# Kernel optimization log

Hardware: AMD Instinct MI355X
Metric: run time of the kernel (lower is better)

Reference implementation:

```python
import jax, jax.numpy as jnp
import numpy as np

E = 4; NQ = 144; NL = 2; NH = 16; H = 1024; OUT = 4096; TD = 256
NT = 5; NEL = 10; TOPK = 2
STAGE_Q = (64, 48, 32); STAGE_IMG = (256, 256, 256)
B = 8; LV = 576; LP = 192


def setup_inputs():
    key = jax.random.key(0)
    ks = jax.random.split(key, 16)
    rn = lambda k, s, std=0.02: jax.random.normal(k, s, jnp.float32) * std
    return dict(
        image_embs=jax.random.normal(ks[0], (B, LV, H), jnp.float32),
        physical_prompts=jax.random.normal(ks[1], (B, LP, H), jnp.float32),
        task_ids=jax.random.randint(ks[2], (B,), 0, NT),
        element_ids=jax.random.randint(ks[3], (B,), 0, NEL),
        query=rn(ks[4], (E, NQ, H), 0.01),
        ln1_w=jnp.ones((E, NL, H)), ln1_b=jnp.zeros((E, NL, H)),
        ln1kv_w=jnp.ones((E, NL, H)), ln1kv_b=jnp.zeros((E, NL, H)),
        attn_in_w=rn(ks[5], (E, NL, 3 * H, H)), attn_in_b=jnp.zeros((E, NL, 3 * H)),
        attn_out_w=rn(ks[6], (E, NL, H, H)), attn_out_b=jnp.zeros((E, NL, H)),
        ls1=jnp.full((E, NL, H), 0.1), ls2=jnp.full((E, NL, H), 0.1),
        ln2_w=jnp.ones((E, NL, H)), ln2_b=jnp.zeros((E, NL, H)),
        fc_w=rn(ks[7], (E, NL, 4 * H, H)), fc_b=jnp.zeros((E, NL, 4 * H)),
        proj_w=rn(ks[8], (E, NL, H, 4 * H)), proj_b=jnp.zeros((E, NL, H)),
        outp_w=rn(ks[9], (E, OUT, H)), outp_b=jnp.zeros((E, OUT)),
        task_emb=rn(ks[10], (NT, TD)), elem_emb=rn(ks[11], (NEL, TD)),
        gate_ln_w=jnp.ones((H + 2 * TD,)), gate_ln_b=jnp.zeros((H + 2 * TD,)),
        gate_w=rn(ks[12], (E, H + 2 * TD)), gate_b=jnp.zeros((E,)),
        output_gain=jnp.full((OUT,), 0.3), final_w=jnp.ones((OUT,)),
    )


def _ln(x, w, b, eps=1e-5):
    m = jnp.mean(x, -1, keepdims=True)
    v = jnp.mean((x - m) ** 2, -1, keepdims=True)
    return (x - m) * jax.lax.rsqrt(v + eps) * w + b


def _mha(q, kv, in_w, in_b, out_w, out_b):
    # torch nn.MultiheadAttention with packed in_proj_weight [3H,H]
    d = q.shape[-1]; hd = d // NH
    qp = (q @ in_w[:d].T + in_b[:d]).reshape(q.shape[0], q.shape[1], NH, hd)
    kp = (kv @ in_w[d:2 * d].T + in_b[d:2 * d]).reshape(kv.shape[0], kv.shape[1], NH, hd)
    vp = (kv @ in_w[2 * d:].T + in_b[2 * d:]).reshape(kv.shape[0], kv.shape[1], NH, hd)
    s = jnp.einsum('bqhd,bkhd->bhqk', qp, kp) / np.float32(np.sqrt(hd))
    a = jax.nn.softmax(s, axis=-1)
    o = jnp.einsum('bhqk,bkhd->bqhd', a, vp).reshape(q.shape)
    return o @ out_w.T + out_b


def _pooler(p, z):
    # One AttnPooler expert. z: [B, LV+LP, H]; stages use fixed query/kv splits.
    b = z.shape[0]
    qt = jnp.broadcast_to(p['query'][None], (b, NQ, H))
    qo = 0; io = 0; outs = []
    for sq, si in zip(STAGE_Q, STAGE_IMG):
        x = qt[:, qo:qo + sq]
        kv0 = jnp.concatenate([x, z[:, io:io + si]], axis=1)  # cat_embs fixed across layers
        qo += sq; io += si
        for l in range(NL):
            kvn = _ln(kv0, p['ln1kv_w'][l], p['ln1kv_b'][l])
            a = _mha(_ln(x, p['ln1_w'][l], p['ln1_b'][l]), kvn,
                     p['attn_in_w'][l], p['attn_in_b'][l],
                     p['attn_out_w'][l], p['attn_out_b'][l])
            x = x + p['ls1'][l] * a
            h = _ln(x, p['ln2_w'][l], p['ln2_b'][l])
            h = jax.nn.gelu(h @ p['fc_w'][l].T + p['fc_b'][l], approximate=False)
            x = x + p['ls2'][l] * (h @ p['proj_w'][l].T + p['proj_b'][l])
        outs.append(x)
    y = jnp.concatenate(outs, axis=1)  # [B, NQ, H]
    return y @ p['outp_w'].T + p['outp_b']  # [B, NQ, OUT]


def reference(image_embs, physical_prompts, task_ids, element_ids, query,
              ln1_w, ln1_b, ln1kv_w, ln1kv_b, attn_in_w, attn_in_b,
              attn_out_w, attn_out_b, ls1, ls2, ln2_w, ln2_b, fc_w, fc_b,
              proj_w, proj_b, outp_w, outp_b, task_emb, elem_emb,
              gate_ln_w, gate_ln_b, gate_w, gate_b, output_gain, final_w):
    # Gating
    tg = jnp.take(task_emb, task_ids, axis=0)
    eg = jnp.take(elem_emb, element_ids, axis=0)
    gi = jnp.concatenate([jnp.mean(image_embs, axis=1), tg, eg], axis=-1)
    logits = jnp.clip(_ln(gi, gate_ln_w, gate_ln_b) @ gate_w.T + gate_b, -15.0, 15.0)
    gw = jax.nn.softmax(logits, axis=-1)
    tw, ti = jax.lax.top_k(gw, TOPK)
    tw = tw / (jnp.sum(tw, axis=-1, keepdims=True) + 1e-9)
    gates = jnp.sum(tw[..., None] * jax.nn.one_hot(ti, E, dtype=tw.dtype), axis=1)  # [B,E]
    # Joint feature sequence
    z = jnp.concatenate([image_embs, physical_prompts], axis=1)
    ep = dict(query=query, ln1_w=ln1_w, ln1_b=ln1_b, ln1kv_w=ln1kv_w, ln1kv_b=ln1kv_b,
              attn_in_w=attn_in_w, attn_in_b=attn_in_b, attn_out_w=attn_out_w,
              attn_out_b=attn_out_b, ls1=ls1, ls2=ls2, ln2_w=ln2_w, ln2_b=ln2_b,
              fc_w=fc_w, fc_b=fc_b, proj_w=proj_w, proj_b=proj_b,
              outp_w=outp_w, outp_b=outp_b)
    eo = jax.vmap(lambda p: _pooler(p, z))(ep)  # [E,B,NQ,OUT]
    comb = jnp.einsum('ebqd,be->bqd', eo, gates)
    rms = comb * jax.lax.rsqrt(jnp.mean(comb * comb, axis=-1, keepdims=True) + 1e-6)
    return rms * final_w * output_gain
```

## Files before the change

### kernel.cpp

```cpp
#include <hip/hip_runtime.h>

typedef unsigned short u16;
typedef __bf16 bf16x8 __attribute__((ext_vector_type(8)));
typedef float f32x4 __attribute__((ext_vector_type(4)));

typedef const __attribute__((address_space(1))) void* gp1;
typedef __attribute__((address_space(3))) void* lp3;

__device__ __forceinline__ float bf2f(u16 u){
    union { unsigned int i; float f; } v; v.i = ((unsigned int)u) << 16; return v.f;
}
__device__ __forceinline__ u16 f2bf(float f){
    union { float f; unsigned int i; } v; v.f = f;
    unsigned int u = v.i;
    return (u16)((u + 0x7FFFu + ((u >> 16) & 1u)) >> 16);
}

__device__ __forceinline__ void gload16(const u16* g, const u16* l){
    __builtin_amdgcn_global_load_lds((gp1)(uintptr_t)g, (lp3)(uintptr_t)l, 16, 0, 0);
}

__device__ __forceinline__ float blockSum(float v){
    #pragma unroll
    for (int off = 32; off; off >>= 1) v += __shfl_xor(v, off, 64);
    __shared__ float sm[4];
    const int w = threadIdx.x >> 6;
    __syncthreads();
    if ((threadIdx.x & 63) == 0) sm[w] = v;
    __syncthreads();
    return sm[0] + sm[1] + sm[2] + sm[3];
}

__global__ __launch_bounds__(256)
void cvt_k(const float* __restrict__ in, u16* __restrict__ out, long long n)
{
    const long long stride = (long long)gridDim.x * 256 * 8;
    for (long long i = ((long long)blockIdx.x * 256 + threadIdx.x) * 8; i < n; i += stride) {
        float4 a = *(const float4*)(in + i);
        float4 b = *(const float4*)(in + i + 4);
        uint4 o;
        o.x = (unsigned)f2bf(a.x) | ((unsigned)f2bf(a.y) << 16);
        o.y = (unsigned)f2bf(a.z) | ((unsigned)f2bf(a.w) << 16);
        o.z = (unsigned)f2bf(b.x) | ((unsigned)f2bf(b.y) << 16);
        o.w = (unsigned)f2bf(b.z) | ((unsigned)f2bf(b.w) << 16);
        *(uint4*)(out + i) = o;
    }
}

__global__ __launch_bounds__(256)
void img_mean_k(const float* __restrict__ img, float* __restrict__ part)
{
    const int b = blockIdx.x >> 5, c = blockIdx.x & 31;
    const int t = threadIdx.x;
    const float* p = img + ((size_t)b * 576 + (size_t)c * 18) * 1024 + t * 4;
    float4 s = make_float4(0.f, 0.f, 0.f, 0.f);
    #pragma unroll
    for (int r = 0; r < 18; r++) {
        float4 v = *(const float4*)(p + (size_t)r * 1024);
        s.x += v.x; s.y += v.y; s.z += v.z; s.w += v.w;
    }
    *(float4*)(part + (size_t)blockIdx.x * 1024 + t * 4) = s;
}

template<int EPI, int TM>
__global__ __launch_bounds__(256)
void gemm_big(const u16* __restrict__ A, long long a_zo, long long a_zi, int lda,
              const u16* __restrict__ W, long long w_zo, long long w_zi, int ldw,
              void* __restrict__ Cv, long long c_zo, long long c_zi, int ldc,
              const float* __restrict__ bias, long long b_zo,
              const float* __restrict__ ls, long long ls_zo,
              int M, int N, int K, int Zi)
{
    constexpr int MI = TM / 32;
    __shared__ u16 As[TM * 64];
    __shared__ u16 Ws[128 * 64];
    const int z  = blockIdx.z;
    const int zo = z / Zi, zi = z - zo * Zi;
    const u16* Az = A + (long long)zo * a_zo + (long long)zi * a_zi;
    const u16* Wz = W + (long long)zo * w_zo + (long long)zi * w_zi;
    const int m0 = blockIdx.y * TM, n0 = blockIdx.x * 128;
    const int t = threadIdx.x;
    const int lane = t & 63, wid = t >> 6;
    const int wm = (wid >> 1) * (TM / 2), wn = (wid & 1) * 64;
    const int qd = lane >> 4, ml = lane & 15;
    const int srow = t >> 3, scol = (t & 7) * 8;

    f32x4 acc[MI][4];
    #pragma unroll
    for (int i = 0; i < MI; i++)
        #pragma unroll
        for (int j = 0; j < 4; j++) acc[i][j] = (f32x4){0.f, 0.f, 0.f, 0.f};

    int arow[MI];
    #pragma unroll
    for (int i = 0; i < MI; i++) {
        int r = m0 + i * 32 + srow; arow[i] = (r < M) ? r : (M - 1);
    }
    int wrow[4];
    #pragma unroll
    for (int i = 0; i < 4; i++) {
        int r = n0 + i * 32 + srow; wrow[i] = (r < N) ? r : (N - 1);
    }

    for (int k0 = 0; k0 < K; k0 += 64) {
        #pragma unroll
        for (int i = 0; i < MI; i++)
            gload16(Az + (size_t)arow[i] * lda + k0 + scol, &As[(i * 32 + wid * 8) * 64]);
        #pragma unroll
        for (int i = 0; i < 4; i++)
            gload16(Wz + (size_t)wrow[i] * ldw + k0 + scol, &Ws[(i * 32 + wid * 8) * 64]);
        __syncthreads();
        #pragma unroll
        for (int kk = 0; kk < 64; kk += 32) {
            bf16x8 af[MI], bfr[4];
            #pragma unroll
            for (int i = 0; i < MI; i++)
                af[i] = __builtin_bit_cast(bf16x8, *(const uint4*)&As[(wm + 16*i + ml) * 64 + kk + qd * 8]);
            #pragma unroll
            for (int j = 0; j < 4; j++)
                bfr[j] = __builtin_bit_cast(bf16x8, *(const uint4*)&Ws[(wn + 16*j + ml) * 64 + kk + qd * 8]);
            #pragma unroll
            for (int i = 0; i < MI; i++)
                #pragma unroll
                for (int j = 0; j < 4; j++)
                    acc[i][j] = __builtin_amdgcn_mfma_f32_16x16x32_bf16(af[i], bfr[j], acc[i][j], 0, 0, 0);
        }
        __syncthreads();
    }

    const float* bz = bias ? bias + (long long)zo * b_zo : nullptr;
    const float* lz = (EPI == 3) ? ls + (long long)zo * ls_zo : nullptr;
    const long long coff = (long long)zo * c_zo + (long long)zi * c_zi;

    #pragma unroll
    for (int i = 0; i < MI; i++) {
        #pragma unroll
        for (int j = 0; j < 4; j++) {
            const int nn = n0 + wn + 16 * j + ml;
            if (nn >= N) continue;
            const float bv = bz ? bz[nn] : 0.f;
            if (EPI == 2) {
                const int mmb = m0 + wm + 16 * i + qd * 4;
                u16* C = (u16*)Cv + coff + (size_t)nn * ldc + mmb;
                if (mmb + 3 < M) {
                    u16 tmp[4];
                    #pragma unroll
                    for (int r = 0; r < 4; r++) tmp[r] = f2bf(acc[i][j][r] + bv);
                    *(uint2*)C = make_uint2((unsigned)tmp[0] | ((unsigned)tmp[1] << 16),
                                            (unsigned)tmp[2] | ((unsigned)tmp[3] << 16));
                } else {
                    #pragma unroll
                    for (int r = 0; r < 4; r++)
                        if (mmb + r < M) C[r] = f2bf(acc[i][j][r] + bv);
                }
            } else {
                const float lsv = (EPI == 3) ? lz[nn] : 0.f;
                #pragma unroll
                for (int r = 0; r < 4; r++) {
                    const int mm = m0 + wm + 16 * i + qd * 4 + r;
                    if (mm >= M) continue;
                    float v = acc[i][j][r];
                    if (EPI == 0) {
                        ((u16*)Cv + coff)[(size_t)mm * ldc + nn] = f2bf(v + bv);
                    } else if (EPI == 3) {
                        float* C = (float*)Cv + coff;
                        const size_t idx = (size_t)mm * ldc + nn;
                        C[idx] = C[idx] + lsv * (v + bv);
                    } else {
                        float x = v + bv;
                        float g = 0.5f * x * (1.f + erff(x * 0.70710678118654752f));
                        ((u16*)Cv + coff)[(size_t)mm * ldc + nn] = f2bf(g);
                    }
                }
            }
        }
    }
}

template<int EPI, int WF32>
__global__ __launch_bounds__(256)
void gemm_k(const u16* __restrict__ A, long long a_zo, long long a_zi, int lda,
            const void* __restrict__ W, long long w_zo, long long w_zi, int ldw,
            void* __restrict__ Cv, long long c_zo, long long c_zi, int ldc,
            const float* __restrict__ bias, long long b_zo,
            const float* __restrict__ ls, long long ls_zo,
            int M, int N, int K, int Zi)
{
    __shared__ u16 As[64][72];
    __shared__ u16 Ws[64][72];
    const int z  = blockIdx.z;
    const int zo = z / Zi, zi = z - zo * Zi;
    const u16* Az = A + (long long)zo * a_zo + (long long)zi * a_zi;
    const long long wbase = (long long)zo * w_zo + (long long)zi * w_zi;
    const int m0 = blockIdx.y * 64, n0 = blockIdx.x * 64;
    const int t = threadIdx.x;
    const int lrow = t >> 2, lcol = (t & 3) * 16;
    const int lane = t & 63, wid = t >> 6;
    const int wm = (wid >> 1) * 32, wn = (wid & 1) * 32;
    const int qd = lane >> 4, ml = lane & 15;

    f32x4 acc[2][2];
    #pragma unroll
    for (int i = 0; i < 2; i++)
        #pragma unroll
        for (int j = 0; j < 2; j++) acc[i][j] = (f32x4){0.f, 0.f, 0.f, 0.f};

    const bool arv = (m0 + lrow) < M;
    const bool wrv = (n0 + lrow) < N;
    const u16* ap = Az + (size_t)(m0 + lrow) * lda + lcol;

    for (int k0 = 0; k0 < K; k0 += 64) {
        {
            uint4 av0 = make_uint4(0u,0u,0u,0u), av1 = make_uint4(0u,0u,0u,0u);
            if (arv && (k0 + lcol) < K) {
                av0 = *(const uint4*)(ap + k0);
                av1 = *(const uint4*)(ap + k0 + 8);
            }
            *(uint4*)&As[lrow][lcol]     = av0;
            *(uint4*)&As[lrow][lcol + 8] = av1;
        }
        if (WF32) {
            const float* wp = (const float*)W + wbase + (size_t)(n0 + lrow) * ldw + lcol;
            const bool ok = wrv && (k0 + lcol) < K;
            u16 tmp[16];
            #pragma unroll
            for (int c = 0; c < 16; c += 4) {
                float4 f = make_float4(0.f,0.f,0.f,0.f);
                if (ok) f = *(const float4*)(wp + k0 + c);
                tmp[c+0] = f2bf(f.x); tmp[c+1] = f2bf(f.y);
                tmp[c+2] = f2bf(f.z); tmp[c+3] = f2bf(f.w);
            }
            unsigned pk[8];
            #pragma unroll
            for (int c = 0; c < 8; c++)
                pk[c] = (unsigned)tmp[2*c] | ((unsigned)tmp[2*c+1] << 16);
            *(uint4*)&Ws[lrow][lcol]     = make_uint4(pk[0],pk[1],pk[2],pk[3]);
            *(uint4*)&Ws[lrow][lcol + 8] = make_uint4(pk[4],pk[5],pk[6],pk[7]);
        } else {
            const u16* wp = (const u16*)W + wbase + (size_t)(n0 + lrow) * ldw + lcol;
            uint4 wv0 = make_uint4(0u,0u,0u,0u), wv1 = make_uint4(0u,0u,0u,0u);
            if (wrv && (k0 + lcol) < K) {
                wv0 = *(const uint4*)(wp + k0);
                wv1 = *(const uint4*)(wp + k0 + 8);
            }
            *(uint4*)&Ws[lrow][lcol]     = wv0;
            *(uint4*)&Ws[lrow][lcol + 8] = wv1;
        }
        __syncthreads();
        #pragma unroll
        for (int kk = 0; kk < 64; kk += 32) {
            bf16x8 af[2], bfr[2];
            #pragma unroll
            for (int i = 0; i < 2; i++) {
                af[i]  = __builtin_bit_cast(bf16x8, *(const uint4*)&As[wm + 16*i + ml][kk + qd*8]);
                bfr[i] = __builtin_bit_cast(bf16x8, *(const uint4*)&Ws[wn + 16*i + ml][kk + qd*8]);
            }
            #pragma unroll
            for (int i = 0; i < 2; i++)
                #pragma unroll
                for (int j = 0; j < 2; j++)
                    acc[i][j] = __builtin_amdgcn_mfma_f32_16x16x32_bf16(af[i], bfr[j], acc[i][j], 0, 0, 0);
        }
        __syncthreads();
    }

    const float* bz = (EPI != 1 && bias) ? bias + (long long)zo * b_zo : nullptr;
    const float* lz = (EPI == 3) ? ls + (long long)zo * ls_zo : nullptr;

    #pragma unroll
    for (int i = 0; i < 2; i++) {
        #pragma unroll
        for (int j = 0; j < 2; j++) {
            const int nn = n0 + wn + 16*j + ml;
            if (nn >= N) continue;
            float bv = 0.f;
            if (EPI != 1 && bz) bv = bz[nn];
            float lsv = 0.f;
            if (EPI == 3) lsv = lz[nn];
            #pragma unroll
            for (int r = 0; r < 4; r++) {
                const int mm = m0 + wm + 16*i + qd*4 + r;
                if (mm >= M) continue;
                float v = acc[i][j][r];
                if (EPI == 0) {
                    u16* C = (u16*)Cv + (long long)zo * c_zo + (long long)zi * c_zi;
                    C[(size_t)mm * ldc + nn] = f2bf(v + bv);
                } else if (EPI == 1) {
                    float* C = (float*)Cv + (long long)zo * c_zo + (long long)zi * c_zi;
                    C[(size_t)mm * ldc + nn] = v * 0.125f;
                } else if (EPI == 2) {
                    u16* C = (u16*)Cv + (long long)zo * c_zo + (long long)zi * c_zi;
                    C[(size_t)nn * ldc + mm] = f2bf(v + bv);
                } else if (EPI == 3) {
                    float* C = (float*)Cv + (long long)zo * c_zo + (long long)zi * c_zi;
                    const size_t idx = (size_t)mm * ldc + nn;
                    C[idx] = C[idx] + lsv * (v + bv);
                } else {
                    u16* C = (u16*)Cv + (long long)zo * c_zo + (long long)zi * c_zi;
                    float x = v + bv;
                    float g = 0.5f * x * (1.f + erff(x * 0.70710678118654752f));
                    C[(size_t)mm * ldc + nn] = f2bf(g);
                }
            }
        }
    }
}

template<int INF32>
__global__ __launch_bounds__(256)
void ln_k(const void* __restrict__ in, u16* __restrict__ out,
          const float* __restrict__ w, const float* __restrict__ b,
          long long wz, int rows_per_e)
{
    const int row = blockIdx.x;
    const int e = row / rows_per_e;
    const int t = threadIdx.x;
    float x[4];
    if (INF32) {
        const float* p = (const float*)in + (size_t)row * 1024;
        #pragma unroll
        for (int j = 0; j < 4; j++) x[j] = p[t + 256*j];
    } else {
        const u16* p = (const u16*)in + (size_t)row * 1024;
        #pragma unroll
        for (int j = 0; j < 4; j++) x[j] = bf2f(p[t + 256*j]);
    }
    float s = x[0] + x[1] + x[2] + x[3];
    s = blockSum(s);
    const float m = s * (1.f / 1024.f);
    float vs = 0.f;
    #pragma unroll
    for (int j = 0; j < 4; j++) { float d = x[j] - m; vs += d * d; }
    vs = blockSum(vs);
    const float rs = rsqrtf(vs * (1.f / 1024.f) + 1e-5f);
    const float* we = w + (long long)e * wz;
    const float* be = b + (long long)e * wz;
    u16* o = out + (size_t)row * 1024;
    #pragma unroll
    for (int j = 0; j < 4; j++) {
        const int h = t + 256*j;
        o[h] = f2bf((x[j] - m) * rs * we[h] + be[h]);
    }
}

__global__ __launch_bounds__(256)
void softmax_k(const float* __restrict__ S, u16* __restrict__ P, int kl, int nrows)
{
    const int r = blockIdx.x * 4 + (threadIdx.x >> 6);
    const int lane = threadIdx.x & 63;
    if (r >= nrows) return;
    const float* s = S + (size_t)r * kl;
    float v[6];
    int cnt = 0;
    float mx = -3.4e38f;
    for (int i = lane; i < kl; i += 64) { float tv = s[i]; v[cnt++] = tv; mx = fmaxf(mx, tv); }
    #pragma unroll
    for (int off = 32; off; off >>= 1) mx = fmaxf(mx, __shfl_xor(mx, off, 64));
    float sum = 0.f;
    for (int i = 0; i < cnt; i++) { v[i] = expf(v[i] - mx); sum += v[i]; }
    #pragma unroll
    for (int off = 32; off; off >>= 1) sum += __shfl_xor(sum, off, 64);
    const float inv = 1.f / sum;
    u16* p = P + (size_t)r * kl;
    cnt = 0;
    for (int i = lane; i < kl; i += 64) p[i] = f2bf(v[cnt++] * inv);
}

__global__ __launch_bounds__(256)
void prep_k(const float* __restrict__ query, const float* __restrict__ img, const float* __restrict__ prm,
            u16* __restrict__ KV0, float* __restrict__ X,
            int sq, int qo, int io, int kl)
{
    const int idx = blockIdx.x;
    const int e = idx / (8 * kl);
    const int rem = idx - e * 8 * kl;
    const int b = rem / kl;
    const int k = rem - b * kl;
    const int t = threadIdx.x;
    const float* src;
    if (k < sq) src = query + ((size_t)e * 144 + qo + k) * 1024;
    else {
        const int zr = io + (k - sq);
        src = (zr < 576) ? img + ((size_t)b * 576 + zr) * 1024
                         : prm + ((size_t)b * 192 + (zr - 576)) * 1024;
    }
    const float4 d = *(const float4*)(src + t * 4);
    u16* dst = KV0 + (((size_t)(e * 8 + b) * kl) + k) * 1024 + t * 4;
    unsigned p0 = (unsigned)f2bf(d.x) | ((unsigned)f2bf(d.y) << 16);
    unsigned p1 = (unsigned)f2bf(d.z) | ((unsigned)f2bf(d.w) << 16);
    *(uint2*)dst = make_uint2(p0, p1);
    if (k < sq) {
        float* xd = X + (((size_t)(e * 8 + b) * sq) + k) * 1024 + t * 4;
        *(float4*)xd = d;
    }
}

__global__ __launch_bounds__(256)
void copy_y_k(const float* __restrict__ X, u16* __restrict__ Y, int sq, int qoff)
{
    const int idx = blockIdx.x;
    const int e = idx / (8 * sq);
    const int rem = idx - e * 8 * sq;
    const int b = rem / sq;
    const int q = rem - b * sq;
    const int t = threadIdx.x;
    const float* xs = X + (((size_t)(e * 8 + b) * sq) + q) * 1024;
    u16* yd = Y + (((size_t)(e * 8 + b) * 144) + qoff + q) * 1024;
    #pragma unroll
    for (int j = 0; j < 4; j++) { const int h = t + 256*j; yd[h] = f2bf(xs[h]); }
}

__global__ __launch_bounds__(256)
void gate_k(const float* __restrict__ part, const int* __restrict__ tids, const int* __restrict__ eids,
            const float* __restrict__ temb, const float* __restrict__ eemb,
            const float* __restrict__ glw, const float* __restrict__ glb,
            const float* __restrict__ gw, const float* __restrict__ gb,
            float* __restrict__ gates)
{
    const int b = blockIdx.x;
    const int t = threadIdx.x;
    __shared__ float gi[1536];
    for (int h = t; h < 1024; h += 256) {
        float s = 0.f;
        #pragma unroll
        for (int c = 0; c < 32; c++) s += part[((size_t)b * 32 + c) * 1024 + h];
        gi[h] = s * (1.f / 576.f);
    }
    {
        const int ti = tids[b], ei = eids[b];
        gi[1024 + t] = temb[ti * 256 + t];
        gi[1280 + t] = eemb[ei * 256 + t];
    }
    __syncthreads();
    float s = 0.f;
    for (int i = t; i < 1536; i += 256) s += gi[i];
    s = blockSum(s);
    const float m = s * (1.f / 1536.f);
    float vs = 0.f;
    for (int i = t; i < 1536; i += 256) { float d = gi[i] - m; vs += d * d; }
    vs = blockSum(vs);
    const float rs = rsqrtf(vs * (1.f / 1536.f) + 1e-5f);
    __shared__ float logit[4];
    for (int e = 0; e < 4; e++) {
        float p = 0.f;
        for (int i = t; i < 1536; i += 256)
            p += ((gi[i] - m) * rs * glw[i] + glb[i]) * gw[e * 1536 + i];
        p = blockSum(p);
        if (t == 0) logit[e] = p + gb[e];
    }
    __syncthreads();
    if (t == 0) {
        float lg[4], ex[4];
        float mx = -1e30f;
        for (int e = 0; e < 4; e++) { lg[e] = fminf(15.f, fmaxf(-15.f, logit[e])); mx = fmaxf(mx, lg[e]); }
        float sum = 0.f;
        for (int e = 0; e < 4; e++) { ex[e] = expf(lg[e] - mx); sum += ex[e]; }
        for (int e = 0; e < 4; e++) ex[e] /= sum;
        int i1 = 0;
        for (int e = 1; e < 4; e++) if (ex[e] > ex[i1]) i1 = e;
        int i2 = -1;
        for (int e = 0; e < 4; e++) if (e != i1 && (i2 < 0 || ex[e] > ex[i2])) i2 = e;
        const float denom = ex[i1] + ex[i2] + 1e-9f;
        float g[4] = {0.f, 0.f, 0.f, 0.f};
        g[i1] = ex[i1] / denom;
        g[i2] = ex[i2] / denom;
        for (int e = 0; e < 4; e++) gates[b * 4 + e] = g[e];
    }
}

__global__ __launch_bounds__(256)
void comb_k(const u16* __restrict__ EO, const float* __restrict__ gates,
            const float* __restrict__ fw, const float* __restrict__ og,
            float* __restrict__ out)
{
    const int bq = blockIdx.x;
    const int b = bq / 144;
    const int t = threadIdx.x;
    float g[4];
    #pragma unroll
    for (int e = 0; e < 4; e++) g[e] = gates[b * 4 + e];
    float c[16];
    float ss = 0.f;
    #pragma unroll
    for (int j = 0; j < 16; j++) {
        const int o = t + 256 * j;
        float v = 0.f;
        #pragma unroll
        for (int e = 0; e < 4; e++)
            v += g[e] * bf2f(EO[((size_t)e * 1152 + bq) * 4096 + o]);
        c[j] = v;
        ss += v * v;
    }
    ss = blockSum(ss);
    const float rs = rsqrtf(ss * (1.f / 4096.f) + 1e-6f);
    #pragma unroll
    for (int j = 0; j < 16; j++) {
        const int o = t + 256 * j;
        out[(size_t)bq * 4096 + o] = c[j] * rs * fw[o] * og[o];
    }
}

extern "C" void kernel_launch(void* const* d_in, const int* in_sizes, int n_in,
                              void* d_out, int out_size, void* d_ws, size_t ws_size,
                              hipStream_t stream)
{
    const float* img  = (const float*)d_in[0];
    const float* prm  = (const float*)d_in[1];
    const int*   tids = (const int*)d_in[2];
    const int*   eids = (const int*)d_in[3];
    const float* query= (const float*)d_in[4];
    const float* ln1w = (const float*)d_in[5];
    const float* ln1b = (const float*)d_in[6];
    const float* lkw  = (const float*)d_in[7];
    const float* lkb  = (const float*)d_in[8];
    const float* aiw  = (const float*)d_in[9];
    const float* aib  = (const float*)d_in[10];
    const float* aow  = (const float*)d_in[11];
    const float* aob  = (const float*)d_in[12];
    const float* ls1  = (const float*)d_in[13];
    const float* ls2  = (const float*)d_in[14];
    const float* l2w  = (const float*)d_in[15];
    const float* l2b  = (const float*)d_in[16];
    const float* fcw  = (const float*)d_in[17];
    const float* fcb  = (const float*)d_in[18];
    const float* pjw  = (const float*)d_in[19];
    const float* pjb  = (const float*)d_in[20];
    const float* opw  = (const float*)d_in[21];
    const float* opb  = (const float*)d_in[22];
    const float* temb = (const float*)d_in[23];
    const float* eemb = (const float*)d_in[24];
    const float* glw  = (const float*)d_in[25];
    const float* glb  = (const float*)d_in[26];
    const float* gww  = (const float*)d_in[27];
    const float* gbb  = (const float*)d_in[28];
    const float* og   = (const float*)d_in[29];
    const float* fwv  = (const float*)d_in[30];
    float* out = (float*)d_out;
    (void)in_sizes; (void)n_in; (void)out_size; (void)ws_size;

    char* ws = (char*)d_ws;
    size_t off = 0;
    auto alloc = [&](size_t bytes) -> char* {
        char* p = ws + off;
        off += (bytes + 255) & ~(size_t)255;
        return p;
    };
    float* GATES = (float*)alloc(128);
    float* IPART = (float*)alloc(1048576);
    u16*  AIWB = (u16*) alloc(50331648);
    u16*  AOWB = (u16*) alloc(16777216);
    u16*  FCWB = (u16*) alloc(67108864);
    u16*  PJWB = (u16*) alloc(67108864);
    u16*  OPWB = (u16*) alloc(33554432);
    u16*  KV0 = (u16*) alloc(20971520);
    u16*  KVN = (u16*) alloc(20971520);
    u16*  KP  = (u16*) alloc(20971520);
    u16*  VT  = (u16*) alloc(20971520);
    float* S  = (float*)alloc(41943040);
    u16*  QN  = (u16*) alloc(4194304);
    u16*  QP  = (u16*) alloc(4194304);
    u16*  AO  = (u16*) alloc(4194304);
    float* X  = (float*)alloc(8388608);
    u16*  H4  = (u16*) alloc(16777216);
    u16*  Y   = (u16*) alloc(9437184);
    u16*  EO  = (u16*) alloc(37748736);

    const long long HH = 1024LL * 1024LL;

    cvt_k<<<2048, 256, 0, stream>>>(aiw, AIWB, 25165824LL);
    cvt_k<<<2048, 256, 0, stream>>>(aow, AOWB, 8388608LL);
    cvt_k<<<2048, 256, 0, stream>>>(fcw, FCWB, 33554432LL);
    cvt_k<<<2048, 256, 0, stream>>>(pjw, PJWB, 33554432LL);
    cvt_k<<<2048, 256, 0, stream>>>(opw, OPWB, 16777216LL);

    img_mean_k<<<256, 256, 0, stream>>>(img, IPART);
    gate_k<<<8, 256, 0, stream>>>(IPART, tids, eids, temb, eemb, glw, glb, gww, gbb, GATES);

    const int SQ[3] = {64, 48, 32};
    const int IO[3] = {0, 256, 512};
    const int QO[3] = {0, 64, 112};
    const int KL[3] = {320, 304, 288};

    for (int s = 0; s < 3; s++) {
        const int sq = SQ[s], kl = KL[s], qo = QO[s], io = IO[s];
        const int Msq = 8 * sq;
        const int Mkl = 8 * kl;
        prep_k<<<4 * 8 * kl, 256, 0, stream>>>(query, img, prm, KV0, X, sq, qo, io, kl);
        for (int l = 0; l < 2; l++) {
            ln_k<0><<<4 * 8 * kl, 256, 0, stream>>>(KV0, KVN, lkw + l*1024, lkb + l*1024, 2048, 8 * kl);
            ln_k<1><<<4 * 8 * sq, 256, 0, stream>>>(X,   QN,  ln1w + l*1024, ln1b + l*1024, 2048, 8 * sq);
            gemm_big<0,64><<<dim3(8, Msq/64, 4), 256, 0, stream>>>(
                QN, (long long)Msq * 1024, 0, 1024,
                AIWB + (long long)l * 3 * HH, 6 * HH, 0, 1024,
                QP, (long long)Msq * 1024, 0, 1024,
                aib + l * 3072, 6144,
                nullptr, 0, Msq, 1024, 1024, 1);
            gemm_big<0,128><<<dim3(8, Mkl/128, 4), 256, 0, stream>>>(
                KVN, (long long)Mkl * 1024, 0, 1024,
                AIWB + (long long)l * 3 * HH + HH, 6 * HH, 0, 1024,
                KP, (long long)Mkl * 1024, 0, 1024,
                aib + l * 3072 + 1024, 6144,
                nullptr, 0, Mkl, 1024, 1024, 1);
            gemm_big<2,128><<<dim3(8, (kl + 127)/128, 32), 256, 0, stream>>>(
                KVN, (long long)8 * kl * 1024, (long long)kl * 1024, 1024,
                AIWB + (long long)l * 3 * HH + 2 * HH, 6 * HH, 0, 1024,
                VT, (long long)8 * 1024 * kl, (long long)1024 * kl, kl,
                aib + l * 3072 + 2048, 6144,
                nullptr, 0, kl, 1024, 1024, 8);
            gemm_k<1,0><<<dim3((kl + 63)/64, 1, 512), 256, 0, stream>>>(
                QP, (long long)sq * 1024, 64, 1024,
                KP, (long long)kl * 1024, 64, 1024,
                S, (long long)16 * sq * kl, (long long)sq * kl, kl,
                nullptr, 0, nullptr, 0, sq, kl, 64, 16);
            {
                const int nrows = 4 * 8 * 16 * sq;
                softmax_k<<<(nrows + 3)/4, 256, 0, stream>>>(S, KVN, kl, nrows);
            }
            gemm_k<0,0><<<dim3(1, 1, 512), 256, 0, stream>>>(
                KVN, (long long)16 * sq * kl, (long long)sq * kl, kl,
                VT, (long long)1024 * kl, (long long)64 * kl, kl,
                AO, (long long)sq * 1024, 64, 1024,
                nullptr, 0, nullptr, 0, sq, 64, kl, 16);
            gemm_big<3,64><<<dim3(8, Msq/64, 4), 256, 0, stream>>>(
                AO, (long long)Msq * 1024, 0, 1024,
                AOWB + (long long)l * HH, 2 * HH, 0, 1024,
                X, (long long)Msq * 1024, 0, 1024,
                aob + l * 1024, 2048,
                ls1 + l * 1024, 2048,
                Msq, 1024, 1024, 1);
            ln_k<1><<<4 * 8 * sq, 256, 0, stream>>>(X, QN, l2w + l*1024, l2b + l*1024, 2048, 8 * sq);
            gemm_big<4,128><<<dim3(32, Msq/128, 4), 256, 0, stream>>>(
                QN, (long long)Msq * 1024, 0, 1024,
                FCWB + (long long)l * 4 * HH, 8 * HH, 0, 1024,
                H4, (long long)Msq * 4096, 0, 4096,
                fcb + l * 4096, 8192,
                nullptr, 0, Msq, 4096, 1024, 1);
            gemm_big<3,64><<<dim3(8, Msq/64, 4), 256, 0, stream>>>(
                H4, (long long)Msq * 4096, 0, 4096,
                PJWB + (long long)l * 4 * HH, 8 * HH, 0, 4096,
                X, (long long)Msq * 1024, 0, 1024,
                pjb + l * 1024, 2048,
                ls2 + l * 1024, 2048,
                Msq, 1024, 4096, 1);
        }
        copy_y_k<<<4 * 8 * sq, 256, 0, stream>>>(X, Y, sq, qo);
    }
    gemm_big<0,128><<<dim3(32, 9, 4), 256, 0, stream>>>(
        Y, 1152LL * 1024, 0, 1024,
        OPWB, 4096LL * 1024, 0, 1024,
        EO, 1152LL * 4096, 0, 4096,
        opb, 4096,
        nullptr, 0, 1152, 4096, 1024, 1);
    comb_k<<<1152, 256, 0, stream>>>(EO, GATES, fwv, og, out);
}
```

Before: 2.964 ms.

## Double-buffer and swizzle gemm_big LDS, fuse K and V projections into one GEMM

gemm_big now double-buffers its LDS tiles so the global-to-LDS loads for the next K-slice overlap the MFMA work on the current one. It also XOR-swizzles the LDS column layout to cut bank conflicts on fragment reads. The separate K-projection and transposed V-projection launches become a single N=2048 GEMM whose new epilogue (EPI 5) writes KP row-major and VT transposed per batch. Dead epilogue branches and the fp32-weight path in gemm_k are removed; the trade-off is double the LDS per block, which can lower occupancy, and the fused epilogue writes without bounds checks, so it relies on Mkl being a multiple of the tile size.

```diff
diff --git a/kernel.cpp b/kernel.cpp
--- a/kernel.cpp
+++ b/kernel.cpp
@@ -72,8 +72,8 @@
               int M, int N, int K, int Zi)
 {
     constexpr int MI = TM / 32;
-    __shared__ u16 As[TM * 64];
-    __shared__ u16 Ws[128 * 64];
+    __shared__ u16 As[2][TM * 64];
+    __shared__ u16 Ws[2][128 * 64];
     const int z  = blockIdx.z;
     const int zo = z / Zi, zi = z - zo * Zi;
     const u16* Az = A + (long long)zo * a_zo + (long long)zi * a_zi;
@@ -83,7 +83,8 @@
     const int lane = t & 63, wid = t >> 6;
     const int wm = (wid >> 1) * (TM / 2), wn = (wid & 1) * 64;
     const int qd = lane >> 4, ml = lane & 15;
-    const int srow = t >> 3, scol = (t & 7) * 8;
+    const int srow = t >> 3;
+    const int scol = (((t & 7) ^ (srow & 7)) << 3);
 
     f32x4 acc[MI][4];
     #pragma unroll
@@ -102,23 +103,37 @@
         int r = n0 + i * 32 + srow; wrow[i] = (r < N) ? r : (N - 1);
     }
 
-    for (int k0 = 0; k0 < K; k0 += 64) {
+    auto stage = [&](int buf, int k0){
         #pragma unroll
         for (int i = 0; i < MI; i++)
-            gload16(Az + (size_t)arow[i] * lda + k0 + scol, &As[(i * 32 + wid * 8) * 64]);
+            gload16(Az + (size_t)arow[i] * lda + k0 + scol, &As[buf][(i * 32 + wid * 8) * 64]);
         #pragma unroll
         for (int i = 0; i < 4; i++)
-            gload16(Wz + (size_t)wrow[i] * ldw + k0 + scol, &Ws[(i * 32 + wid * 8) * 64]);
-        __syncthreads();
+            gload16(Wz + (size_t)wrow[i] * ldw + k0 + scol, &Ws[buf][(i * 32 + wid * 8) * 64]);
+    };
+
+    const int NT = K >> 6;
+    stage(0, 0);
+    __syncthreads();
+    for (int it = 0; it < NT; ++it) {
+        if (it + 1 < NT) stage((it + 1) & 1, (it + 1) << 6);
+        const u16* Ab = As[it & 1];
+        const u16* Wb = Ws[it & 1];
         #pragma unroll
         for (int kk = 0; kk < 64; kk += 32) {
             bf16x8 af[MI], bfr[4];
             #pragma unroll
-            for (int i = 0; i < MI; i++)
-                af[i] = __builtin_bit_cast(bf16x8, *(const uint4*)&As[(wm + 16*i + ml) * 64 + kk + qd * 8]);
-            #pragma unroll
-            for (int j = 0; j < 4; j++)
-                bfr[j] = __builtin_bit_cast(bf16x8, *(const uint4*)&Ws[(wn + 16*j + ml) * 64 + kk + qd * 8]);
+            for (int i = 0; i < MI; i++) {
+                const int row = wm + 16 * i + ml;
+                const int ch  = (((qd + (kk >> 3)) ^ (ml & 7)) << 3);
+                af[i] = __builtin_bit_cast(bf16x8, *(const uint4*)&Ab[row * 64 + ch]);
+            }
+            #pragma unroll
+            for (int j = 0; j < 4; j++) {
+                const int row = wn + 16 * j + ml;
+                const int ch  = (((qd + (kk >> 3)) ^ (ml & 7)) << 3);
+                bfr[j] = __builtin_bit_cast(bf16x8, *(const uint4*)&Wb[row * 64 + ch]);
+            }
             #pragma unroll
             for (int i = 0; i < MI; i++)
                 #pragma unroll
@@ -132,6 +147,36 @@
     const float* lz = (EPI == 3) ? ls + (long long)zo * ls_zo : nullptr;
     const long long coff = (long long)zo * c_zo + (long long)zi * c_zi;
 
+    if (EPI == 5) {
+        const int klv = (int)c_zi;
+        u16* KPz = (u16*)Cv + (long long)zo * c_zo;
+        u16* VTz = (u16*)(uintptr_t)(const void*)ls + (long long)zo * ls_zo;
+        #pragma unroll
+        for (int i = 0; i < MI; i++) {
+            #pragma unroll
+            for (int j = 0; j < 4; j++) {
+                const int nn = n0 + wn + 16 * j + ml;
+                const float bv = bz[nn];
+                const int mmb = m0 + wm + 16 * i + qd * 4;
+                if (nn < 1024) {
+                    #pragma unroll
+                    for (int r = 0; r < 4; r++)
+                        KPz[(size_t)(mmb + r) * ldc + nn] = f2bf(acc[i][j][r] + bv);
+                } else {
+                    const int b = mmb / klv;
+                    const int k = mmb - b * klv;
+                    u16 tmp[4];
+                    #pragma unroll
+                    for (int r = 0; r < 4; r++) tmp[r] = f2bf(acc[i][j][r] + bv);
+                    u16* p = VTz + ((size_t)(b * 1024 + (nn - 1024))) * klv + k;
+                    *(uint2*)p = make_uint2((unsigned)tmp[0] | ((unsigned)tmp[1] << 16),
+                                            (unsigned)tmp[2] | ((unsigned)tmp[3] << 16));
+                }
+            }
+        }
+        return;
+    }
+
     #pragma unroll
     for (int i = 0; i < MI; i++) {
         #pragma unroll
@@ -139,38 +184,22 @@
             const int nn = n0 + wn + 16 * j + ml;
             if (nn >= N) continue;
             const float bv = bz ? bz[nn] : 0.f;
-            if (EPI == 2) {
-                const int mmb = m0 + wm + 16 * i + qd * 4;
-                u16* C = (u16*)Cv + coff + (size_t)nn * ldc + mmb;
-                if (mmb + 3 < M) {
-                    u16 tmp[4];
-                    #pragma unroll
-                    for (int r = 0; r < 4; r++) tmp[r] = f2bf(acc[i][j][r] + bv);
-                    *(uint2*)C = make_uint2((unsigned)tmp[0] | ((unsigned)tmp[1] << 16),
-                                            (unsigned)tmp[2] | ((unsigned)tmp[3] << 16));
+            const float lsv = (EPI == 3) ? lz[nn] : 0.f;
+            #pragma unroll
+            for (int r = 0; r < 4; r++) {
+                const int mm = m0 + wm + 16 * i + qd * 4 + r;
+                if (mm >= M) continue;
+                float v = acc[i][j][r];
+                if (EPI == 0) {
+                    ((u16*)Cv + coff)[(size_t)mm * ldc + nn] = f2bf(v + bv);
+                } else if (EPI == 3) {
+                    float* C = (float*)Cv + coff;
+                    const size_t idx = (size_t)mm * ldc + nn;
+                    C[idx] = C[idx] + lsv * (v + bv);
                 } else {
-                    #pragma unroll
-                    for (int r = 0; r < 4; r++)
-                        if (mmb + r < M) C[r] = f2bf(acc[i][j][r] + bv);
-                }
-            } else {
-                const float lsv = (EPI == 3) ? lz[nn] : 0.f;
-                #pragma unroll
-                for (int r = 0; r < 4; r++) {
-                    const int mm = m0 + wm + 16 * i + qd * 4 + r;
-                    if (mm >= M) continue;
-                    float v = acc[i][j][r];
-                    if (EPI == 0) {
-                        ((u16*)Cv + coff)[(size_t)mm * ldc + nn] = f2bf(v + bv);
-                    } else if (EPI == 3) {
-                        float* C = (float*)Cv + coff;
-                        const size_t idx = (size_t)mm * ldc + nn;
-                        C[idx] = C[idx] + lsv * (v + bv);
-                    } else {
-                        float x = v + bv;
-                        float g = 0.5f * x * (1.f + erff(x * 0.70710678118654752f));
-                        ((u16*)Cv + coff)[(size_t)mm * ldc + nn] = f2bf(g);
-                    }
+                    float x = v + bv;
+                    float g = 0.5f * x * (1.f + erff(x * 0.70710678118654752f));
+                    ((u16*)Cv + coff)[(size_t)mm * ldc + nn] = f2bf(g);
                 }
             }
         }
@@ -219,24 +248,7 @@
             *(uint4*)&As[lrow][lcol]     = av0;
             *(uint4*)&As[lrow][lcol + 8] = av1;
         }
-        if (WF32) {
-            const float* wp = (const float*)W + wbase + (size_t)(n0 + lrow) * ldw + lcol;
-            const bool ok = wrv && (k0 + lcol) < K;
-            u16 tmp[16];
-            #pragma unroll
-            for (int c = 0; c < 16; c += 4) {
-                float4 f = make_float4(0.f,0.f,0.f,0.f);
-                if (ok) f = *(const float4*)(wp + k0 + c);
-                tmp[c+0] = f2bf(f.x); tmp[c+1] = f2bf(f.y);
-                tmp[c+2] = f2bf(f.z); tmp[c+3] = f2bf(f.w);
-            }
-            unsigned pk[8];
-            #pragma unroll
-            for (int c = 0; c < 8; c++)
-                pk[c] = (unsigned)tmp[2*c] | ((unsigned)tmp[2*c+1] << 16);
-            *(uint4*)&Ws[lrow][lcol]     = make_uint4(pk[0],pk[1],pk[2],pk[3]);
-            *(uint4*)&Ws[lrow][lcol + 8] = make_uint4(pk[4],pk[5],pk[6],pk[7]);
-        } else {
+        {
             const u16* wp = (const u16*)W + wbase + (size_t)(n0 + lrow) * ldw + lcol;
             uint4 wv0 = make_uint4(0u,0u,0u,0u), wv1 = make_uint4(0u,0u,0u,0u);
             if (wrv && (k0 + lcol) < K) {
@@ -264,42 +276,23 @@
         __syncthreads();
     }
 
-    const float* bz = (EPI != 1 && bias) ? bias + (long long)zo * b_zo : nullptr;
-    const float* lz = (EPI == 3) ? ls + (long long)zo * ls_zo : nullptr;
-
     #pragma unroll
     for (int i = 0; i < 2; i++) {
         #pragma unroll
         for (int j = 0; j < 2; j++) {
             const int nn = n0 + wn + 16*j + ml;
             if (nn >= N) continue;
-            float bv = 0.f;
-            if (EPI != 1 && bz) bv = bz[nn];
-            float lsv = 0.f;
-            if (EPI == 3) lsv = lz[nn];
             #pragma unroll
             for (int r = 0; r < 4; r++) {
                 const int mm = m0 + wm + 16*i + qd*4 + r;
                 if (mm >= M) continue;
                 float v = acc[i][j][r];
-                if (EPI == 0) {
-                    u16* C = (u16*)Cv + (long long)zo * c_zo + (long long)zi * c_zi;
-                    C[(size_t)mm * ldc + nn] = f2bf(v + bv);
-                } else if (EPI == 1) {
+                if (EPI == 1) {
                     float* C = (float*)Cv + (long long)zo * c_zo + (long long)zi * c_zi;
                     C[(size_t)mm * ldc + nn] = v * 0.125f;
-                } else if (EPI == 2) {
-                    u16* C = (u16*)Cv + (long long)zo * c_zo + (long long)zi * c_zi;
-                    C[(size_t)nn * ldc + mm] = f2bf(v + bv);
-                } else if (EPI == 3) {
-                    float* C = (float*)Cv + (long long)zo * c_zo + (long long)zi * c_zi;
-                    const size_t idx = (size_t)mm * ldc + nn;
-                    C[idx] = C[idx] + lsv * (v + bv);
                 } else {
                     u16* C = (u16*)Cv + (long long)zo * c_zo + (long long)zi * c_zi;
-                    float x = v + bv;
-                    float g = 0.5f * x * (1.f + erff(x * 0.70710678118654752f));
-                    C[(size_t)mm * ldc + nn] = f2bf(g);
+                    C[(size_t)mm * ldc + nn] = f2bf(v);
                 }
             }
         }
@@ -595,18 +588,13 @@
                 QP, (long long)Msq * 1024, 0, 1024,
                 aib + l * 3072, 6144,
                 nullptr, 0, Msq, 1024, 1024, 1);
-            gemm_big<0,128><<<dim3(8, Mkl/128, 4), 256, 0, stream>>>(
+            gemm_big<5,128><<<dim3(16, Mkl/128, 4), 256, 0, stream>>>(
                 KVN, (long long)Mkl * 1024, 0, 1024,
                 AIWB + (long long)l * 3 * HH + HH, 6 * HH, 0, 1024,
-                KP, (long long)Mkl * 1024, 0, 1024,
+                KP, (long long)Mkl * 1024,  (long long)kl, 1024,
                 aib + l * 3072 + 1024, 6144,
-                nullptr, 0, Mkl, 1024, 1024, 1);
-            gemm_big<2,128><<<dim3(8, (kl + 127)/128, 32), 256, 0, stream>>>(
-                KVN, (long long)8 * kl * 1024, (long long)kl * 1024, 1024,
-                AIWB + (long long)l * 3 * HH + 2 * HH, 6 * HH, 0, 1024,
-                VT, (long long)8 * 1024 * kl, (long long)1024 * kl, kl,
-                aib + l * 3072 + 2048, 6144,
-                nullptr, 0, kl, 1024, 1024, 8);
+                (const float*)VT, (long long)8 * 1024 * kl,
+                Mkl, 2048, 1024, 1);
             gemm_k<1,0><<<dim3((kl + 63)/64, 1, 512), 256, 0, stream>>>(
                 QP, (long long)sq * 1024, 64, 1024,
                 KP, (long long)kl * 1024, 64, 1024,
```

New measurement: 2.393 ms. 1.24x faster.
